# Optimization experiments

Hardware: AMD Instinct MI355X
Metric: run time of the kernel (lower is better)

The kernel has to match this reference:

```python
import jax, jax.numpy as jnp
import numpy as np

N_NODES = 4096
N_SUBS = 1024
NUM_FEATURES = 128
HIDDEN = 512
NHEADS = 8
DHEAD = HIDDEN // NHEADS
NUM_LAYERS = 2
EDGE_PROB = 0.01
NEG_INF = -1e9


def _make_adj(key, n, p):
    a = (jax.random.uniform(key, (n, n)) < p).astype(jnp.float32)
    return jnp.maximum(a, jnp.eye(n, dtype=jnp.float32))  # self-loops


def setup_inputs() -> dict:
    key = jax.random.key(0)
    ks = jax.random.split(key, 12)
    x = jax.random.normal(ks[0], (N_NODES, NUM_FEATURES), dtype=jnp.float32)
    adj_node = _make_adj(ks[1], N_NODES, EDGE_PROB)
    adj_substation = _make_adj(ks[2], N_SUBS, 4 * EDGE_PROB)
    seg_ids = jnp.sort(jax.random.randint(ks[3], (N_NODES,), 0, N_SUBS, dtype=jnp.int32))
    s = 0.05
    lin_w = jax.random.normal(ks[4], (NUM_FEATURES, HIDDEN), dtype=jnp.float32) * s
    lin_b = jnp.zeros((HIDDEN,), dtype=jnp.float32)
    node_W = jax.random.normal(ks[5], (NUM_LAYERS, HIDDEN, HIDDEN), dtype=jnp.float32) * s
    node_asrc = jax.random.normal(ks[6], (NUM_LAYERS, NHEADS, DHEAD), dtype=jnp.float32) * s
    node_adst = jax.random.normal(ks[7], (NUM_LAYERS, NHEADS, DHEAD), dtype=jnp.float32) * s
    sub_W = jax.random.normal(ks[8], (NUM_LAYERS, HIDDEN, HIDDEN), dtype=jnp.float32) * s
    sub_asrc = jax.random.normal(ks[9], (NUM_LAYERS, NHEADS, DHEAD), dtype=jnp.float32) * s
    sub_adst = jax.random.normal(ks[10], (NUM_LAYERS, NHEADS, DHEAD), dtype=jnp.float32) * s
    return {"x": x, "adj_node": adj_node, "adj_substation": adj_substation,
            "seg_ids": seg_ids, "lin_w": lin_w, "lin_b": lin_b,
            "node_W": node_W, "node_asrc": node_asrc, "node_adst": node_adst,
            "sub_W": sub_W, "sub_asrc": sub_asrc, "sub_adst": sub_adst}


def _gat_layer(h, adj, W, a_src, a_dst):
    # h: [N, F]; adj: [N, N]; W: [F, F]; a_src/a_dst: [H, Dh]
    n = h.shape[0]
    Wh = (h @ W).reshape(n, NHEADS, DHEAD)               # [N, H, Dh]
    f_src = jnp.einsum('nhd,hd->hn', Wh, a_src)          # [H, N]
    f_dst = jnp.einsum('nhd,hd->hn', Wh, a_dst)          # [H, N]
    e = jax.nn.leaky_relu(f_src[:, :, None] + f_dst[:, None, :], 0.2)  # [H, N, N]
    e = jnp.where(adj[None] > 0, e, NEG_INF)
    alpha = jax.nn.softmax(e, axis=-1)                   # [H, N, N]
    out = jnp.einsum('hij,jhd->ihd', alpha, Wh).reshape(n, NHEADS * DHEAD)
    return jax.nn.elu(out)


def _stacked_gats(h, adj, Ws, asrcs, adsts):
    # Faithful to the source bug: x is never rebound, each layer sees the
    # original input; the last layer's output is returned.
    out = h
    for i in range(Ws.shape[0]):
        out = _gat_layer(h, adj, Ws[i], asrcs[i], adsts[i])
    return out


def _pool_mean(h, seg_ids, num_segments):
    sums = jax.ops.segment_sum(h, seg_ids, num_segments=num_segments)
    counts = jax.ops.segment_sum(jnp.ones((h.shape[0], 1), h.dtype), seg_ids,
                                 num_segments=num_segments)
    return sums / jnp.maximum(counts, 1.0)


def reference(x, adj_node, adj_substation, seg_ids, lin_w, lin_b,
              node_W, node_asrc, node_adst, sub_W, sub_asrc, sub_adst):
    h = x @ lin_w + lin_b                                  # [N, HIDDEN]
    h = _stacked_gats(h, adj_node, node_W, node_asrc, node_adst)
    s = _pool_mean(h, seg_ids, N_SUBS)                     # [S, HIDDEN]
    s = _stacked_gats(s, adj_substation, sub_W, sub_asrc, sub_adst)
    return s
```

## Files before the change

kernel.cpp:

```cpp
#include <hip/hip_runtime.h>
#include <hip/hip_bf16.h>
#include <hip/hip_fp16.h>
#include <math.h>

#define N_NODES 4096
#define N_SUBS  1024
#define NFEAT   128
#define HIDDEN  512
#define NHEADS  8
#define DHEAD   64
#define CAP     128
#define ROWG    4
#define HGS     8

typedef float vfloat4 __attribute__((ext_vector_type(4)));

struct alignas(16) h8 { __half2 a, b, c, d; };

#define NB_EXTRACT (N_NODES / 4 + N_SUBS / 4)
#define NB_GEMM    (8 * 3 * 16)
#define BM 64
#define BN 64
#define BK 16

__global__ __launch_bounds__(256) void phase1(const float* __restrict__ adj_n,
                                              const float* __restrict__ adj_s,
                                              int* __restrict__ cnt_n,
                                              int* __restrict__ nbr_n,
                                              int* __restrict__ cnt_s,
                                              int* __restrict__ nbr_s,
                                              const float* __restrict__ lin_w,
                                              const float* __restrict__ node_W1,
                                              const float* __restrict__ lin_b,
                                              float* __restrict__ Wpart,
                                              float* __restrict__ bpart) {
    const int tid = threadIdx.x;
    if (blockIdx.x < NB_EXTRACT) {
        const int w = tid >> 6;
        const int lane = tid & 63;
        const float* adj;
        int N, row;
        int* cnt;
        int* nbr;
        if (blockIdx.x < N_NODES / 4) {
            adj = adj_n; N = N_NODES; cnt = cnt_n; nbr = nbr_n;
            row = blockIdx.x * 4 + w;
        } else {
            adj = adj_s; N = N_SUBS; cnt = cnt_s; nbr = nbr_s;
            row = (blockIdx.x - N_NODES / 4) * 4 + w;
        }
        const vfloat4* rowp = (const vfloat4*)(adj + (size_t)row * N);
        int* nrow = nbr + (row << 7);
        const int n4 = N >> 2;
        int c = 0;
        const unsigned long long below = (1ull << lane) - 1ull;
        for (int c4 = lane; c4 < n4; c4 += 64) {
            const vfloat4 v = __builtin_nontemporal_load(&rowp[c4]);
            const int col = c4 << 2;
            unsigned long long m;
            bool p;
            p = v.x > 0.0f; m = __ballot(p);
            if (p) { int q = c + __popcll(m & below); if (q < CAP) nrow[q] = col; }
            c += __popcll(m);
            p = v.y > 0.0f; m = __ballot(p);
            if (p) { int q = c + __popcll(m & below); if (q < CAP) nrow[q] = col + 1; }
            c += __popcll(m);
            p = v.z > 0.0f; m = __ballot(p);
            if (p) { int q = c + __popcll(m & below); if (q < CAP) nrow[q] = col + 2; }
            c += __popcll(m);
            p = v.w > 0.0f; m = __ballot(p);
            if (p) { int q = c + __popcll(m & below); if (q < CAP) nrow[q] = col + 3; }
            c += __popcll(m);
        }
        if (lane == 0) cnt[row] = c < CAP ? c : CAP;
        return;
    }
    {
        const int b = blockIdx.x - NB_EXTRACT;
        const int bn = (b & 7) * BN;
        const int rem = b >> 3;
        const int by = rem % 3;
        const int bz = rem / 3;
        const int M = NFEAT, N = HIDDEN, K = HIDDEN;
        const int k_chunk = K / 16;
        const int k_start = bz * k_chunk;
        __shared__ float As[BK][BM + 4];
        __shared__ float Bs[BK][BN + 4];
        if (by == 2) {
            const int q = tid >> 6;
            const int n = tid & 63;
            const int sub = k_chunk >> 2;
            const int kb = k_start + q * sub;
            float s = 0.0f;
            for (int k = 0; k < sub; k++)
                s += lin_b[kb + k] * node_W1[(size_t)(kb + k) * N + bn + n];
            float* red = (float*)As;
            red[q * 64 + n] = s;
            __syncthreads();
            if (q == 0)
                bpart[bz * N + bn + n] = red[n] + red[64 + n] + red[128 + n] + red[192 + n];
            return;
        }
        const int bm = by * BM;
        float* Cw = Wpart + (size_t)bz * M * N;
        const int tr = tid >> 4;
        const int tc = tid & 15;
        const int am = tid >> 2;
        const int ak4 = (tid & 3) * 4;
        const int bk = tid >> 4;
        const int bn0 = (tid & 15) * 4;
        float acc[4][4] = {};
        for (int k0 = k_start; k0 < k_start + k_chunk; k0 += BK) {
            const float4 va = *(const float4*)&lin_w[(size_t)(bm + am) * K + k0 + ak4];
            const float4 vb = *(const float4*)&node_W1[(size_t)(k0 + bk) * N + bn + bn0];
            As[ak4 + 0][am] = va.x;
            As[ak4 + 1][am] = va.y;
            As[ak4 + 2][am] = va.z;
            As[ak4 + 3][am] = va.w;
            *(float4*)&Bs[bk][bn0] = vb;
            __syncthreads();
#pragma unroll
            for (int k = 0; k < BK; k++) {
                const float4 a4 = *(const float4*)&As[k][tr * 4];
                const float4 b4 = *(const float4*)&Bs[k][tc * 4];
                const float a[4] = {a4.x, a4.y, a4.z, a4.w};
                const float bb[4] = {b4.x, b4.y, b4.z, b4.w};
#pragma unroll
                for (int i = 0; i < 4; i++)
#pragma unroll
                    for (int j = 0; j < 4; j++)
                        acc[i][j] += a[i] * bb[j];
            }
            __syncthreads();
        }
#pragma unroll
        for (int i = 0; i < 4; i++) {
            const int m = bm + tr * 4 + i;
            float4 o = {acc[i][0], acc[i][1], acc[i][2], acc[i][3]};
            *(float4*)&Cw[(size_t)m * N + bn + tc * 4] = o;
        }
    }
}

__global__ __launch_bounds__(256) void gemm_f32(const float* __restrict__ A,
                                                const float* __restrict__ B,
                                                const float* __restrict__ bias,
                                                float* __restrict__ C,
                                                int M, int N, int K, int k_chunk,
                                                const float* __restrict__ asrc,
                                                const float* __restrict__ adst,
                                                float* __restrict__ fs,
                                                float* __restrict__ fd,
                                                __half* __restrict__ C_h) {
    __shared__ float As[BK][BM + 4];
    __shared__ float Bs[BK][BN + 4];
    const int tid = threadIdx.x;
    const int bm = blockIdx.y * BM;
    const int bn = blockIdx.x * BN;
    const int k_start = blockIdx.z * k_chunk;
    const int k_end = (k_start + k_chunk) < K ? (k_start + k_chunk) : K;
    float* Cw = C + (size_t)blockIdx.z * M * N;
    const int tr = tid >> 4;
    const int tc = tid & 15;
    const int am = tid >> 2;
    const int ak4 = (tid & 3) * 4;
    const int bk = tid >> 4;
    const int bn0 = (tid & 15) * 4;
    float acc[4][4] = {};
    for (int k0 = k_start; k0 < k_end; k0 += BK) {
        const float4 va = *(const float4*)&A[(size_t)(bm + am) * K + k0 + ak4];
        const float4 vb = *(const float4*)&B[(size_t)(k0 + bk) * N + bn + bn0];
        As[ak4 + 0][am] = va.x;
        As[ak4 + 1][am] = va.y;
        As[ak4 + 2][am] = va.z;
        As[ak4 + 3][am] = va.w;
        *(float4*)&Bs[bk][bn0] = vb;
        __syncthreads();
#pragma unroll
        for (int k = 0; k < BK; k++) {
            const float4 a4 = *(const float4*)&As[k][tr * 4];
            const float4 b4 = *(const float4*)&Bs[k][tc * 4];
            const float a[4] = {a4.x, a4.y, a4.z, a4.w};
            const float b[4] = {b4.x, b4.y, b4.z, b4.w};
#pragma unroll
            for (int i = 0; i < 4; i++)
#pragma unroll
                for (int j = 0; j < 4; j++)
                    acc[i][j] += a[i] * b[j];
        }
        __syncthreads();
    }
#pragma unroll
    for (int i = 0; i < 4; i++) {
        const int m = bm + tr * 4 + i;
        if (bias) {
            const float4 bv = *(const float4*)&bias[bn + tc * 4];
            acc[i][0] += bv.x; acc[i][1] += bv.y; acc[i][2] += bv.z; acc[i][3] += bv.w;
        }
        if (C_h) {
            __half2 p0 = __floats2half2_rn(acc[i][0], acc[i][1]);
            __half2 p1 = __floats2half2_rn(acc[i][2], acc[i][3]);
            __half2* hp = (__half2*)&C_h[(size_t)m * N + bn + tc * 4];
            hp[0] = p0;
            hp[1] = p1;
        } else {
            float4 o = {acc[i][0], acc[i][1], acc[i][2], acc[i][3]};
            *(float4*)&Cw[(size_t)m * N + bn + tc * 4] = o;
        }
    }
    if (asrc) {
        const int h = blockIdx.x;
        const float4 as4 = *(const float4*)&asrc[h * DHEAD + tc * 4];
        const float4 ad4 = *(const float4*)&adst[h * DHEAD + tc * 4];
#pragma unroll
        for (int i = 0; i < 4; i++) {
            float vs = acc[i][0] * as4.x + acc[i][1] * as4.y +
                       acc[i][2] * as4.z + acc[i][3] * as4.w;
            float vd = acc[i][0] * ad4.x + acc[i][1] * ad4.y +
                       acc[i][2] * ad4.z + acc[i][3] * ad4.w;
#pragma unroll
            for (int off = 1; off < 16; off <<= 1) {
                vs += __shfl_xor(vs, off, 64);
                vd += __shfl_xor(vd, off, 64);
            }
            if (tc == 0) {
                const int m = bm + tr * 4 + i;
                fs[h * M + m] = vs;
                fd[h * M + m] = vd;
            }
        }
    }
}

__global__ __launch_bounds__(256) void reduce_both(const float* __restrict__ p1,
                                                   float* __restrict__ o1,
                                                   int len1, int nz1,
                                                   const float* __restrict__ p2,
                                                   float* __restrict__ o2,
                                                   int len2, int nz2,
                                                   int blocks1) {
    if ((int)blockIdx.x < blocks1) {
        const int i = blockIdx.x * 256 + threadIdx.x;
        if (i < len1) {
            float s = 0.0f;
            for (int z = 0; z < nz1; z++) s += p1[(size_t)z * len1 + i];
            o1[i] = s;
        }
    } else {
        const int i = (blockIdx.x - blocks1) * 256 + threadIdx.x;
        if (i < len2) {
            float s = 0.0f;
            for (int z = 0; z < nz2; z++) s += p2[(size_t)z * len2 + i];
            o2[i] = s;
        }
    }
}

__global__ __launch_bounds__(512) void reduce_fsfd(const float* __restrict__ part,
                                                   float* __restrict__ wh,
                                                   const float* __restrict__ asrc,
                                                   const float* __restrict__ adst,
                                                   float* __restrict__ fs,
                                                   float* __restrict__ fd,
                                                   int M, int nz) {
    const int n = blockIdx.x;
    const int tid = threadIdx.x;
    float v = 0.0f;
    for (int z = 0; z < nz; z++)
        v += part[((size_t)z * M + n) * HIDDEN + tid];
    wh[(size_t)n * HIDDEN + tid] = v;
    const int h = tid >> 6;
    const int d = tid & 63;
    float vs = v * asrc[h * DHEAD + d];
    float vd = v * adst[h * DHEAD + d];
#pragma unroll
    for (int off = 32; off >= 1; off >>= 1) {
        vs += __shfl_xor(vs, off, 64);
        vd += __shfl_xor(vd, off, 64);
    }
    if (d == 0) {
        fs[h * M + n] = vs;
        fd[h * M + n] = vd;
    }
}

__device__ __forceinline__ void gat_softmax(const float* __restrict__ fs,
                                            const float* __restrict__ fd,
                                            const int* snbr, float (*ex)[CAP + 1],
                                            int C, int i, int N, int tid) {
    const int h = tid >> 6;
    const int lane = tid & 63;
    const float fsi = fs[h * N + i];
    const float* __restrict__ fdh = fd + h * N;
    float m = -1e30f;
    for (int k = lane; k < C; k += 64) {
        float e = fsi + fdh[snbr[k]];
        e = e > 0.0f ? e : 0.2f * e;
        ex[h][k] = e;
        m = fmaxf(m, e);
    }
#pragma unroll
    for (int off = 32; off >= 1; off >>= 1) m = fmaxf(m, __shfl_xor(m, off, 64));
    float ssum = 0.0f;
    for (int k = lane; k < C; k += 64) {
        float v = __expf(ex[h][k] - m);
        ex[h][k] = v;
        ssum += v;
    }
#pragma unroll
    for (int off = 32; off >= 1; off >>= 1) ssum += __shfl_xor(ssum, off, 64);
    const float inv = 1.0f / ssum;
    for (int k = lane; k < C; k += 64) ex[h][k] *= inv;
}

__global__ __launch_bounds__(512) void gat_agg_h(const __half* __restrict__ Wh,
                                                 const float* __restrict__ fs,
                                                 const float* __restrict__ fd,
                                                 const int* __restrict__ cnt,
                                                 const int* __restrict__ nbr,
                                                 float* __restrict__ out, int N) {
    __shared__ int snbr[CAP];
    __shared__ float ex[NHEADS][CAP + 1];
    __shared__ float sacc[HGS][HIDDEN];
    const int i = blockIdx.x;
    const int tid = threadIdx.x;
    int C = cnt[i];
    C = C < CAP ? C : CAP;
    for (int k = tid; k < C; k += 512) snbr[k] = nbr[(i << 7) + k];
    __syncthreads();
    gat_softmax(fs, fd, snbr, ex, C, i, N, tid);
    __syncthreads();
    const int g = tid >> 6;
    const int t = tid & 63;
    const int hh = t >> 3;
    float a0f[8] = {};
    float* acc = a0f;
    int k = g;
    for (; k + 3 * HGS < C; k += 4 * HGS) {
        const int j0 = snbr[k];
        const int j1 = snbr[k + HGS];
        const int j2 = snbr[k + 2 * HGS];
        const int j3 = snbr[k + 3 * HGS];
        const float a0 = ex[hh][k];
        const float a1 = ex[hh][k + HGS];
        const float a2 = ex[hh][k + 2 * HGS];
        const float a3 = ex[hh][k + 3 * HGS];
        const h8 w0 = *(const h8*)&Wh[(size_t)j0 * HIDDEN + 8 * t];
        const h8 w1 = *(const h8*)&Wh[(size_t)j1 * HIDDEN + 8 * t];
        const h8 w2 = *(const h8*)&Wh[(size_t)j2 * HIDDEN + 8 * t];
        const h8 w3 = *(const h8*)&Wh[(size_t)j3 * HIDDEN + 8 * t];
        float2 f;
        f = __half22float2(w0.a); acc[0] += a0 * f.x; acc[1] += a0 * f.y;
        f = __half22float2(w0.b); acc[2] += a0 * f.x; acc[3] += a0 * f.y;
        f = __half22float2(w0.c); acc[4] += a0 * f.x; acc[5] += a0 * f.y;
        f = __half22float2(w0.d); acc[6] += a0 * f.x; acc[7] += a0 * f.y;
        f = __half22float2(w1.a); acc[0] += a1 * f.x; acc[1] += a1 * f.y;
        f = __half22float2(w1.b); acc[2] += a1 * f.x; acc[3] += a1 * f.y;
        f = __half22float2(w1.c); acc[4] += a1 * f.x; acc[5] += a1 * f.y;
        f = __half22float2(w1.d); acc[6] += a1 * f.x; acc[7] += a1 * f.y;
        f = __half22float2(w2.a); acc[0] += a2 * f.x; acc[1] += a2 * f.y;
        f = __half22float2(w2.b); acc[2] += a2 * f.x; acc[3] += a2 * f.y;
        f = __half22float2(w2.c); acc[4] += a2 * f.x; acc[5] += a2 * f.y;
        f = __half22float2(w2.d); acc[6] += a2 * f.x; acc[7] += a2 * f.y;
        f = __half22float2(w3.a); acc[0] += a3 * f.x; acc[1] += a3 * f.y;
        f = __half22float2(w3.b); acc[2] += a3 * f.x; acc[3] += a3 * f.y;
        f = __half22float2(w3.c); acc[4] += a3 * f.x; acc[5] += a3 * f.y;
        f = __half22float2(w3.d); acc[6] += a3 * f.x; acc[7] += a3 * f.y;
    }
    for (; k < C; k += HGS) {
        const int j0 = snbr[k];
        const float a0 = ex[hh][k];
        const h8 w0 = *(const h8*)&Wh[(size_t)j0 * HIDDEN + 8 * t];
        float2 f;
        f = __half22float2(w0.a); acc[0] += a0 * f.x; acc[1] += a0 * f.y;
        f = __half22float2(w0.b); acc[2] += a0 * f.x; acc[3] += a0 * f.y;
        f = __half22float2(w0.c); acc[4] += a0 * f.x; acc[5] += a0 * f.y;
        f = __half22float2(w0.d); acc[6] += a0 * f.x; acc[7] += a0 * f.y;
    }
    *(float4*)&sacc[g][8 * t] = *(float4*)&acc[0];
    *(float4*)&sacc[g][8 * t + 4] = *(float4*)&acc[4];
    __syncthreads();
    if (g == 0) {
#pragma unroll
        for (int e = 0; e < 8; e++) {
            float r = acc[e];
#pragma unroll
            for (int gg = 1; gg < HGS; gg++) r += sacc[gg][8 * t + e];
            out[(size_t)i * HIDDEN + 8 * t + e] =
                r > 0.0f ? r : __expf(r) - 1.0f;
        }
    }
}

__global__ __launch_bounds__(512) void gat_agg_f(const float* __restrict__ Wh,
                                                 const float* __restrict__ fs,
                                                 const float* __restrict__ fd,
                                                 const int* __restrict__ cnt,
                                                 const int* __restrict__ nbr,
                                                 float* __restrict__ out, int N) {
    __shared__ int snbr[CAP];
    __shared__ float ex[NHEADS][CAP + 1];
    __shared__ float sacc[ROWG][HIDDEN];
    const int i = blockIdx.x;
    const int tid = threadIdx.x;
    int C = cnt[i];
    C = C < CAP ? C : CAP;
    for (int k = tid; k < C; k += 512) snbr[k] = nbr[(i << 7) + k];
    __syncthreads();
    gat_softmax(fs, fd, snbr, ex, C, i, N, tid);
    __syncthreads();
    const int g = tid >> 7;
    const int t = tid & 127;
    const int hh = t >> 4;
    float4 acc = {0.f, 0.f, 0.f, 0.f};
    int k = g;
    for (; k + 3 * ROWG < C; k += 4 * ROWG) {
        const int j0 = snbr[k];
        const int j1 = snbr[k + ROWG];
        const int j2 = snbr[k + 2 * ROWG];
        const int j3 = snbr[k + 3 * ROWG];
        const float a0 = ex[hh][k];
        const float a1 = ex[hh][k + ROWG];
        const float a2 = ex[hh][k + 2 * ROWG];
        const float a3 = ex[hh][k + 3 * ROWG];
        const float4 w0 = *(const float4*)&Wh[(size_t)j0 * HIDDEN + 4 * t];
        const float4 w1 = *(const float4*)&Wh[(size_t)j1 * HIDDEN + 4 * t];
        const float4 w2 = *(const float4*)&Wh[(size_t)j2 * HIDDEN + 4 * t];
        const float4 w3 = *(const float4*)&Wh[(size_t)j3 * HIDDEN + 4 * t];
        acc.x += a0 * w0.x + a1 * w1.x + a2 * w2.x + a3 * w3.x;
        acc.y += a0 * w0.y + a1 * w1.y + a2 * w2.y + a3 * w3.y;
        acc.z += a0 * w0.z + a1 * w1.z + a2 * w2.z + a3 * w3.z;
        acc.w += a0 * w0.w + a1 * w1.w + a2 * w2.w + a3 * w3.w;
    }
    for (; k < C; k += ROWG) {
        const int j0 = snbr[k];
        const float a0 = ex[hh][k];
        const float4 w0 = *(const float4*)&Wh[(size_t)j0 * HIDDEN + 4 * t];
        acc.x += a0 * w0.x; acc.y += a0 * w0.y;
        acc.z += a0 * w0.z; acc.w += a0 * w0.w;
    }
    *(float4*)&sacc[g][4 * t] = acc;
    __syncthreads();
    if (g == 0) {
        float4 r = acc;
#pragma unroll
        for (int gg = 1; gg < ROWG; gg++) {
            const float4 o = *(const float4*)&sacc[gg][4 * t];
            r.x += o.x; r.y += o.y; r.z += o.z; r.w += o.w;
        }
        r.x = r.x > 0.0f ? r.x : __expf(r.x) - 1.0f;
        r.y = r.y > 0.0f ? r.y : __expf(r.y) - 1.0f;
        r.z = r.z > 0.0f ? r.z : __expf(r.z) - 1.0f;
        r.w = r.w > 0.0f ? r.w : __expf(r.w) - 1.0f;
        *(float4*)&out[(size_t)i * HIDDEN + 4 * t] = r;
    }
}

__global__ __launch_bounds__(512) void pool_kernel(const float* __restrict__ hin,
                                                   const int* __restrict__ seg,
                                                   float* __restrict__ sout) {
    const int s = blockIdx.x;
    const int d = threadIdx.x;
    int lo = 0, hi = N_NODES;
    while (lo < hi) { int mid = (lo + hi) >> 1; if (seg[mid] < s) lo = mid + 1; else hi = mid; }
    const int start = lo;
    hi = N_NODES;
    while (lo < hi) { int mid = (lo + hi) >> 1; if (seg[mid] < s + 1) lo = mid + 1; else hi = mid; }
    const int end = lo;
    float acc = 0.0f;
    for (int r = start; r < end; r++) acc += hin[(size_t)r * HIDDEN + d];
    const int c = end - start;
    sout[(size_t)s * HIDDEN + d] = acc / (c > 0 ? (float)c : 1.0f);
}

extern "C" void kernel_launch(void* const* d_in, const int* in_sizes, int n_in,
                              void* d_out, int out_size, void* d_ws, size_t ws_size,
                              hipStream_t stream) {
    const float* x        = (const float*)d_in[0];
    const float* adj_node = (const float*)d_in[1];
    const float* adj_sub  = (const float*)d_in[2];
    const int*   seg_ids  = (const int*)d_in[3];
    const float* lin_w    = (const float*)d_in[4];
    const float* lin_b    = (const float*)d_in[5];
    const float* node_W1    = (const float*)d_in[6]  + HIDDEN * HIDDEN;
    const float* node_asrc1 = (const float*)d_in[7]  + NHEADS * DHEAD;
    const float* node_adst1 = (const float*)d_in[8]  + NHEADS * DHEAD;
    const float* sub_W1     = (const float*)d_in[9]  + HIDDEN * HIDDEN;
    const float* sub_asrc1  = (const float*)d_in[10] + NHEADS * DHEAD;
    const float* sub_adst1  = (const float*)d_in[11] + NHEADS * DHEAD;
    float* out = (float*)d_out;

    char* ws = (char*)d_ws;
    float* bufA  = (float*)(ws);
    float* bufB  = (float*)(ws + (size_t)8 * 1024 * 1024);
    float* fs_n  = (float*)(ws + (size_t)16 * 1024 * 1024);
    float* fd_n  = fs_n + NHEADS * N_NODES;
    float* fs_s  = fd_n + NHEADS * N_NODES;
    float* fd_s  = fs_s + NHEADS * N_SUBS;
    int*   cnt_n = (int*)(fd_s + NHEADS * N_SUBS);
    int*   cnt_s = cnt_n + N_NODES;
    int*   nbr_n = cnt_s + N_SUBS;
    int*   nbr_s = nbr_n + N_NODES * CAP;

    float*  Wpart = bufB;
    float*  Wfuse = bufB + 16 * NFEAT * HIDDEN;
    float*  bpart = Wfuse + NFEAT * HIDDEN;
    float*  bias2 = bpart + 16 * HIDDEN;
    float*  gatom = bufB;
    float*  Spart = bufB;
    __half* wh_n  = (__half*)bufA;
    float*  sp    = bufA;
    float*  wh_s  = bufA + (size_t)N_SUBS * HIDDEN;

    phase1<<<NB_EXTRACT + NB_GEMM, 256, 0, stream>>>(
        adj_node, adj_sub, cnt_n, nbr_n, cnt_s, nbr_s,
        lin_w, node_W1, lin_b, Wpart, bpart);
    reduce_both<<<NFEAT * HIDDEN / 256 + 2, 256, 0, stream>>>(
        Wpart, Wfuse, NFEAT * HIDDEN, 16, bpart, bias2, HIDDEN, 16,
        NFEAT * HIDDEN / 256);
    gemm_f32<<<dim3(HIDDEN / BN, N_NODES / BM, 1), 256, 0, stream>>>(
        x, Wfuse, bias2, nullptr, N_NODES, HIDDEN, NFEAT, NFEAT,
        node_asrc1, node_adst1, fs_n, fd_n, wh_n);
    gat_agg_h<<<N_NODES, 512, 0, stream>>>(wh_n, fs_n, fd_n, cnt_n, nbr_n,
                                           gatom, N_NODES);
    pool_kernel<<<N_SUBS, 512, 0, stream>>>(gatom, seg_ids, sp);
    gemm_f32<<<dim3(HIDDEN / BN, N_SUBS / BM, 4), 256, 0, stream>>>(
        sp, sub_W1, nullptr, Spart, N_SUBS, HIDDEN, HIDDEN, HIDDEN / 4,
        nullptr, nullptr, nullptr, nullptr, nullptr);
    reduce_fsfd<<<N_SUBS, 512, 0, stream>>>(Spart, wh_s, sub_asrc1, sub_adst1,
                                            fs_s, fd_s, N_SUBS, 4);
    gat_agg_f<<<N_SUBS, 512, 0, stream>>>(wh_s, fs_s, fd_s, cnt_s, nbr_s,
                                          out, N_SUBS);
}
```

Measured before the change: 206.2 us.

## Map one node per wavefront in fp16 GAT aggregation, dropping block syncs

The node-level GAT aggregation now gives each 64-lane wavefront its own destination node, eight nodes per block, in place of one node per 512-thread block with a shared-memory cross-group reduction. Softmax is computed per wave with 8-lane shuffles, and each lane accumulates 8 output features over all neighbors with an 8-wide unrolled gather, then writes ELU results directly with float4 stores. This removes __syncthreads barriers and the shared-memory partial-sum reduction, and launches far fewer blocks. In exchange, each wave walks the whole neighbor list serially, giving less memory-level parallelism per node.

```diff
diff --git a/kernel.cpp b/kernel.cpp
--- a/kernel.cpp
+++ b/kernel.cpp
@@ -11,7 +11,7 @@
 #define DHEAD   64
 #define CAP     128
 #define ROWG    4
-#define HGS     8
+#define CAPP    (CAP + 4)
 
 typedef float vfloat4 __attribute__((ext_vector_type(4)));
 
@@ -319,77 +319,75 @@
                                                  const int* __restrict__ cnt,
                                                  const int* __restrict__ nbr,
                                                  float* __restrict__ out, int N) {
-    __shared__ int snbr[CAP];
-    __shared__ float ex[NHEADS][CAP + 1];
-    __shared__ float sacc[HGS][HIDDEN];
-    const int i = blockIdx.x;
-    const int tid = threadIdx.x;
+    __shared__ int snbr[8][CAP];
+    __shared__ float al[8][NHEADS][CAPP];
+    const int w = threadIdx.x >> 6;
+    const int lane = threadIdx.x & 63;
+    const int i = blockIdx.x * 8 + w;
     int C = cnt[i];
     C = C < CAP ? C : CAP;
-    for (int k = tid; k < C; k += 512) snbr[k] = nbr[(i << 7) + k];
-    __syncthreads();
-    gat_softmax(fs, fd, snbr, ex, C, i, N, tid);
-    __syncthreads();
-    const int g = tid >> 6;
-    const int t = tid & 63;
-    const int hh = t >> 3;
-    float a0f[8] = {};
-    float* acc = a0f;
-    int k = g;
-    for (; k + 3 * HGS < C; k += 4 * HGS) {
-        const int j0 = snbr[k];
-        const int j1 = snbr[k + HGS];
-        const int j2 = snbr[k + 2 * HGS];
-        const int j3 = snbr[k + 3 * HGS];
-        const float a0 = ex[hh][k];
-        const float a1 = ex[hh][k + HGS];
-        const float a2 = ex[hh][k + 2 * HGS];
-        const float a3 = ex[hh][k + 3 * HGS];
-        const h8 w0 = *(const h8*)&Wh[(size_t)j0 * HIDDEN + 8 * t];
-        const h8 w1 = *(const h8*)&Wh[(size_t)j1 * HIDDEN + 8 * t];
-        const h8 w2 = *(const h8*)&Wh[(size_t)j2 * HIDDEN + 8 * t];
-        const h8 w3 = *(const h8*)&Wh[(size_t)j3 * HIDDEN + 8 * t];
+    for (int k = lane; k < C; k += 64) snbr[w][k] = nbr[(i << 7) + k];
+    const int h = lane >> 3;
+    const int s = lane & 7;
+    const float fsi = fs[h * N + i];
+    const float* __restrict__ fdh = fd + h * N;
+    float m = -1e30f;
+    for (int k = s; k < C; k += 8) {
+        float e = fsi + fdh[snbr[w][k]];
+        e = e > 0.0f ? e : 0.2f * e;
+        al[w][h][k] = e;
+        m = fmaxf(m, e);
+    }
+    m = fmaxf(m, __shfl_xor(m, 1, 64));
+    m = fmaxf(m, __shfl_xor(m, 2, 64));
+    m = fmaxf(m, __shfl_xor(m, 4, 64));
+    float ssum = 0.0f;
+    for (int k = s; k < C; k += 8) {
+        float v = __expf(al[w][h][k] - m);
+        al[w][h][k] = v;
+        ssum += v;
+    }
+    ssum += __shfl_xor(ssum, 1, 64);
+    ssum += __shfl_xor(ssum, 2, 64);
+    ssum += __shfl_xor(ssum, 4, 64);
+    const float inv = 1.0f / ssum;
+    for (int k = s; k < C; k += 8) al[w][h][k] *= inv;
+    float acc[8] = {};
+    int k = 0;
+    for (; k + 8 <= C; k += 8) {
+        h8 ww[8];
+        float aa[8];
+#pragma unroll
+        for (int u = 0; u < 8; u++) {
+            ww[u] = *(const h8*)&Wh[(size_t)snbr[w][k + u] * HIDDEN + 8 * lane];
+            aa[u] = al[w][h][k + u];
+        }
+#pragma unroll
+        for (int u = 0; u < 8; u++) {
+            float2 f;
+            f = __half22float2(ww[u].a); acc[0] += aa[u] * f.x; acc[1] += aa[u] * f.y;
+            f = __half22float2(ww[u].b); acc[2] += aa[u] * f.x; acc[3] += aa[u] * f.y;
+            f = __half22float2(ww[u].c); acc[4] += aa[u] * f.x; acc[5] += aa[u] * f.y;
+            f = __half22float2(ww[u].d); acc[6] += aa[u] * f.x; acc[7] += aa[u] * f.y;
+        }
+    }
+    for (; k < C; k++) {
+        const h8 w0 = *(const h8*)&Wh[(size_t)snbr[w][k] * HIDDEN + 8 * lane];
+        const float a0 = al[w][h][k];
         float2 f;
         f = __half22float2(w0.a); acc[0] += a0 * f.x; acc[1] += a0 * f.y;
         f = __half22float2(w0.b); acc[2] += a0 * f.x; acc[3] += a0 * f.y;
         f = __half22float2(w0.c); acc[4] += a0 * f.x; acc[5] += a0 * f.y;
         f = __half22float2(w0.d); acc[6] += a0 * f.x; acc[7] += a0 * f.y;
-        f = __half22float2(w1.a); acc[0] += a1 * f.x; acc[1] += a1 * f.y;
-        f = __half22float2(w1.b); acc[2] += a1 * f.x; acc[3] += a1 * f.y;
-        f = __half22float2(w1.c); acc[4] += a1 * f.x; acc[5] += a1 * f.y;
-        f = __half22float2(w1.d); acc[6] += a1 * f.x; acc[7] += a1 * f.y;
-        f = __half22float2(w2.a); acc[0] += a2 * f.x; acc[1] += a2 * f.y;
-        f = __half22float2(w2.b); acc[2] += a2 * f.x; acc[3] += a2 * f.y;
-        f = __half22float2(w2.c); acc[4] += a2 * f.x; acc[5] += a2 * f.y;
-        f = __half22float2(w2.d); acc[6] += a2 * f.x; acc[7] += a2 * f.y;
-        f = __half22float2(w3.a); acc[0] += a3 * f.x; acc[1] += a3 * f.y;
-        f = __half22float2(w3.b); acc[2] += a3 * f.x; acc[3] += a3 * f.y;
-        f = __half22float2(w3.c); acc[4] += a3 * f.x; acc[5] += a3 * f.y;
-        f = __half22float2(w3.d); acc[6] += a3 * f.x; acc[7] += a3 * f.y;
-    }
-    for (; k < C; k += HGS) {
-        const int j0 = snbr[k];
-        const float a0 = ex[hh][k];
-        const h8 w0 = *(const h8*)&Wh[(size_t)j0 * HIDDEN + 8 * t];
-        float2 f;
-        f = __half22float2(w0.a); acc[0] += a0 * f.x; acc[1] += a0 * f.y;
-        f = __half22float2(w0.b); acc[2] += a0 * f.x; acc[3] += a0 * f.y;
-        f = __half22float2(w0.c); acc[4] += a0 * f.x; acc[5] += a0 * f.y;
-        f = __half22float2(w0.d); acc[6] += a0 * f.x; acc[7] += a0 * f.y;
-    }
-    *(float4*)&sacc[g][8 * t] = *(float4*)&acc[0];
-    *(float4*)&sacc[g][8 * t + 4] = *(float4*)&acc[4];
-    __syncthreads();
-    if (g == 0) {
-#pragma unroll
-        for (int e = 0; e < 8; e++) {
-            float r = acc[e];
-#pragma unroll
-            for (int gg = 1; gg < HGS; gg++) r += sacc[gg][8 * t + e];
-            out[(size_t)i * HIDDEN + 8 * t + e] =
-                r > 0.0f ? r : __expf(r) - 1.0f;
-        }
-    }
+    }
+#pragma unroll
+    for (int e = 0; e < 8; e++)
+        acc[e] = acc[e] > 0.0f ? acc[e] : __expf(acc[e]) - 1.0f;
+    float4 o0 = {acc[0], acc[1], acc[2], acc[3]};
+    float4 o1 = {acc[4], acc[5], acc[6], acc[7]};
+    float4* op = (float4*)&out[(size_t)i * HIDDEN + 8 * lane];
+    op[0] = o0;
+    op[1] = o1;
 }
 
 __global__ __launch_bounds__(512) void gat_agg_f(const float* __restrict__ Wh,
@@ -521,8 +519,8 @@
     gemm_f32<<<dim3(HIDDEN / BN, N_NODES / BM, 1), 256, 0, stream>>>(
         x, Wfuse, bias2, nullptr, N_NODES, HIDDEN, NFEAT, NFEAT,
         node_asrc1, node_adst1, fs_n, fd_n, wh_n);
-    gat_agg_h<<<N_NODES, 512, 0, stream>>>(wh_n, fs_n, fd_n, cnt_n, nbr_n,
-                                           gatom, N_NODES);
+    gat_agg_h<<<N_NODES / 8, 512, 0, stream>>>(wh_n, fs_n, fd_n, cnt_n, nbr_n,
+                                               gatom, N_NODES);
     pool_kernel<<<N_SUBS, 512, 0, stream>>>(gatom, seg_ids, sp);
     gemm_f32<<<dim3(HIDDEN / BN, N_SUBS / BM, 4), 256, 0, stream>>>(
         sp, sub_W1, nullptr, Spart, N_SUBS, HIDDEN, HIDDEN, HIDDEN / 4,
```

Result: faster. 201.1 us (-2.5%).
